# Optimization experiments

Measured on AMD Instinct MI355X. Metric: run time of the kernel, lower is better.

Reference implementation:

```python
import jax, jax.numpy as jnp
import numpy as np

C = 64
D = C // 8  # query/key channels
B, H, W = 4, 64, 64


def setup_inputs() -> dict:
    key = jax.random.key(0)
    ks = jax.random.split(key, 8)
    x = jax.random.normal(ks[0], (B, C, H, W), dtype=jnp.float32)
    # 1x1 conv params (kernel squeezed to [out_ch, in_ch])
    sq = 1.0 / np.sqrt(C)
    Wq = jax.random.uniform(ks[1], (D, C), jnp.float32, -sq, sq)
    bq = jax.random.uniform(ks[2], (D,), jnp.float32, -sq, sq)
    Wk = jax.random.uniform(ks[3], (D, C), jnp.float32, -sq, sq)
    bk = jax.random.uniform(ks[4], (D,), jnp.float32, -sq, sq)
    Wv = jax.random.uniform(ks[5], (C, C), jnp.float32, -sq, sq)
    bv = jax.random.uniform(ks[6], (C,), jnp.float32, -sq, sq)
    # gamma is zero-initialized in the module; use a nonzero value so the
    # attention path actually contributes to the output.
    gamma = jax.random.normal(ks[7], (1,), dtype=jnp.float32)
    return {"x": x, "Wq": Wq, "bq": bq, "Wk": Wk, "bk": bk, "Wv": Wv, "bv": bv, "gamma": gamma}


def reference(x, Wq, bq, Wk, bk, Wv, bv, gamma):
    b, c, h, w = x.shape
    n = h * w
    xf = x.reshape(b, c, n)                                   # [B,C,N]
    q = jnp.einsum('dc,bcn->bdn', Wq, xf) + bq[None, :, None]  # [B,D,N]
    k = jnp.einsum('dc,bcn->bdn', Wk, xf) + bk[None, :, None]  # [B,D,N]
    v = jnp.einsum('ec,bcn->ben', Wv, xf) + bv[None, :, None]  # [B,C,N]
    energy = jnp.einsum('bdn,bdm->bnm', q, k)                  # [B,N,N] = Q^T K
    attn = jax.nn.softmax(energy, axis=-1)                     # softmax over keys m
    # out[b,c,n] = sum_m v[b,c,m] * attn[b,n,m]  (V @ attention^T in torch)
    out = jnp.einsum('bcm,bnm->bcn', v, attn).reshape(b, c, h, w)
    return gamma[0] * out + x
```

## Files before the change

### kernel.cpp

```cpp
#include <hip/hip_runtime.h>
#include <hip/hip_bf16.h>
#include <math.h>

#define BB 4
#define CC 64
#define DD 8
#define NN 4096
#define KS 8
#define KPS (NN / KS)
#define LOG2E 1.44269504088896340736f

typedef __attribute__((ext_vector_type(4))) short short4v;
typedef __attribute__((ext_vector_type(8))) unsigned short ushort8;
typedef __attribute__((ext_vector_type(16))) float f32x16;

#if defined(__HIP_DEVICE_COMPILE__)
  #if __has_builtin(__builtin_amdgcn_mfma_f32_32x32x8bf16_1k)
    #define MFMA32x8(A, B, C) __builtin_amdgcn_mfma_f32_32x32x8bf16_1k(A, B, C, 0, 0, 0)
  #elif __has_builtin(__builtin_amdgcn_mfma_f32_32x32x8_bf16)
    #define MFMA32x8(A, B, C) __builtin_amdgcn_mfma_f32_32x32x8_bf16(A, B, C, 0, 0, 0)
  #else
    #error "no 32x32x8 bf16 MFMA builtin in device pass"
  #endif
  #if __has_builtin(__builtin_amdgcn_exp2f)
    #define EXP2(x) __builtin_amdgcn_exp2f(x)
  #else
    #define EXP2(x) exp2f(x)
  #endif
#else
  static __device__ __host__ inline f32x16 MFMA32x8(short4v, short4v, f32x16 c) { return c; }
  #define EXP2(x) exp2f(x)
#endif

static __device__ inline short4v pack4(float a, float b, float c, float d) {
    union { short4v s; __hip_bfloat162 h[2]; } u;
    u.h[0] = __float22bfloat162_rn(make_float2(a, b));
    u.h[1] = __float22bfloat162_rn(make_float2(c, d));
    return u.s;
}

__global__ __launch_bounds__(256) void qkv_kernel(
    const float* __restrict__ x,  const float* __restrict__ Wq, const float* __restrict__ bq,
    const float* __restrict__ Wk, const float* __restrict__ bk,
    const float* __restrict__ Wv, const float* __restrict__ bv,
    unsigned short* __restrict__ qb, unsigned short* __restrict__ kb,
    unsigned short* __restrict__ vT)
{
    __shared__ unsigned short LQ[128 * 8];
    __shared__ unsigned short LK[128 * 8];

    int tid = threadIdx.x;
    int wave = tid >> 6, lane = tid & 63;
    int l32 = lane & 31, h2 = lane >> 5;

    int blk = blockIdx.x;
    int b = blk & (BB - 1);
    int r2 = blk >> 2;
    int rt = r2 % 3;
    int ng = r2 / 3;
    int n0 = ng * 128 + wave * 32;

    short4v af[8];
    #pragma unroll
    for (int s = 0; s < 8; ++s) {
        float4 w4;
        if (rt < 2) {
            w4 = *(const float4*)(Wv + (size_t)(rt * 32 + l32) * CC + s * 8 + 4 * h2);
        } else if (l32 < 8) {
            w4 = *(const float4*)(Wq + (size_t)l32 * CC + s * 8 + 4 * h2);
        } else if (l32 < 16) {
            w4 = *(const float4*)(Wk + (size_t)(l32 - 8) * CC + s * 8 + 4 * h2);
        } else {
            w4 = make_float4(0.f, 0.f, 0.f, 0.f);
        }
        af[s] = pack4(w4.x, w4.y, w4.z, w4.w);
    }

    const float* xb = x + (size_t)b * CC * NN + n0 + l32;
    short4v bf[8];
    #pragma unroll
    for (int s = 0; s < 8; ++s) {
        int c0 = s * 8 + 4 * h2;
        float x0 = xb[(size_t)(c0 + 0) * NN];
        float x1 = xb[(size_t)(c0 + 1) * NN];
        float x2 = xb[(size_t)(c0 + 2) * NN];
        float x3 = xb[(size_t)(c0 + 3) * NN];
        bf[s] = pack4(x0, x1, x2, x3);
    }

    f32x16 acc;
    #pragma unroll
    for (int r = 0; r < 16; ++r) acc[r] = 0.f;
    #pragma unroll
    for (int s = 0; s < 8; ++s)
        acc = MFMA32x8(af[s], bf[s], acc);

    if (rt < 2) {
        #pragma unroll
        for (int r = 0; r < 16; ++r) {
            int row = rt * 32 + (r & 3) + 8 * (r >> 2) + 4 * h2;
            float val = acc[r] + bv[row];
            __hip_bfloat16 hv = __float2bfloat16(val);
            vT[((size_t)b * CC + row) * NN + n0 + l32] = *(unsigned short*)&hv;
        }
    } else {
        short4v qp = pack4((acc[0] + bq[0 + 4 * h2]) * LOG2E,
                           (acc[1] + bq[1 + 4 * h2]) * LOG2E,
                           (acc[2] + bq[2 + 4 * h2]) * LOG2E,
                           (acc[3] + bq[3 + 4 * h2]) * LOG2E);
        short4v kp = pack4(acc[4] + bk[0 + 4 * h2],
                           acc[5] + bk[1 + 4 * h2],
                           acc[6] + bk[2 + 4 * h2],
                           acc[7] + bk[3 + 4 * h2]);
        int nl = wave * 32 + l32;
        *(short4v*)(LQ + (size_t)nl * 8 + 4 * h2) = qp;
        *(short4v*)(LK + (size_t)nl * 8 + 4 * h2) = kp;
        __syncthreads();
        if (tid < 128) {
            ushort8 row = *(const ushort8*)(LQ + (size_t)tid * 8);
            *(ushort8*)(qb + ((size_t)b * NN + ng * 128 + tid) * 8) = row;
        } else {
            int t = tid - 128;
            ushort8 row = *(const ushort8*)(LK + (size_t)t * 8);
            *(ushort8*)(kb + ((size_t)b * NN + ng * 128 + t) * 8) = row;
        }
    }
}

__global__ __launch_bounds__(256, 4) void flash_kernel(
    const unsigned short* __restrict__ qb, const unsigned short* __restrict__ kb,
    const unsigned short* __restrict__ vT, float* __restrict__ obuf,
    float* __restrict__ ssb)
{
    __shared__ unsigned short VS[64 * 132];
    int tid = threadIdx.x;
    int wave = tid >> 6, lane = tid & 63;
    int l32 = lane & 31, h2 = lane >> 5;

    int blk = blockIdx.x;
    int b = blk & (BB - 1);
    int rest = blk >> 2;
    int split = rest & (KS - 1);
    int qchunk = rest >> 3;
    int n0 = qchunk * 128 + wave * 32;

    short4v qf = *(const short4v*)(qb + ((size_t)b * NN + n0 + l32) * DD + h2 * 4);

    const unsigned short* kbb = kb + (size_t)b * NN * DD;
    const unsigned short* vbb = vT + (size_t)b * CC * NN;
    int m0 = split * KPS;

    int cch = tid >> 4, kg = tid & 15;
    int kgx = (kg ^ (cch & 3)) * 8;

    f32x16 o0, o1, zz;
    #pragma unroll
    for (int r = 0; r < 16; ++r) { o0[r] = 0.f; o1[r] = 0.f; zz[r] = 0.f; }
    float s0 = 0.f, s1 = 0.f, s2 = 0.f, s3 = 0.f;

    ushort8 vr0 = *(const ushort8*)(vbb + (size_t)(cch)      * NN + m0 + kg * 8);
    ushort8 vr1 = *(const ushort8*)(vbb + (size_t)(16 + cch) * NN + m0 + kg * 8);
    ushort8 vr2 = *(const ushort8*)(vbb + (size_t)(32 + cch) * NN + m0 + kg * 8);
    ushort8 vr3 = *(const ushort8*)(vbb + (size_t)(48 + cch) * NN + m0 + kg * 8);

    for (int tile = 0; tile < 4; ++tile) {
        *(ushort8*)(VS + (size_t)(cch)      * 132 + kgx) = vr0;
        *(ushort8*)(VS + (size_t)(16 + cch) * 132 + kgx) = vr1;
        *(ushort8*)(VS + (size_t)(32 + cch) * 132 + kgx) = vr2;
        *(ushort8*)(VS + (size_t)(48 + cch) * 132 + kgx) = vr3;
        __syncthreads();

        if (tile < 3) {
            int mn = m0 + (tile + 1) * 128;
            vr0 = *(const ushort8*)(vbb + (size_t)(cch)      * NN + mn + kg * 8);
            vr1 = *(const ushort8*)(vbb + (size_t)(16 + cch) * NN + mn + kg * 8);
            vr2 = *(const ushort8*)(vbb + (size_t)(32 + cch) * NN + mn + kg * 8);
            vr3 = *(const ushort8*)(vbb + (size_t)(48 + cch) * NN + mn + kg * 8);
        }

        short4v kf[4];
        #pragma unroll
        for (int s = 0; s < 4; ++s)
            kf[s] = *(const short4v*)(kbb + (size_t)(m0 + tile * 128 + s * 32 + l32) * DD + h2 * 4);

        #pragma unroll
        for (int sub = 0; sub < 4; ++sub) {
            f32x16 st = MFMA32x8(kf[sub], qf, zz);
            float w[16];
            #pragma unroll
            for (int r = 0; r < 16; ++r) w[r] = EXP2(st[r]);
            s0 += (w[0] + w[1]) + (w[2] + w[3]);
            s1 += (w[4] + w[5]) + (w[6] + w[7]);
            s2 += (w[8] + w[9]) + (w[10] + w[11]);
            s3 += (w[12] + w[13]) + (w[14] + w[15]);

            union { short4v s; __hip_bfloat162 h[2]; } u[4];
            #pragma unroll
            for (int g = 0; g < 4; ++g) {
                u[g].h[0] = __float22bfloat162_rn(make_float2(w[4 * g],     w[4 * g + 1]));
                u[g].h[1] = __float22bfloat162_rn(make_float2(w[4 * g + 2], w[4 * g + 3]));
            }
            #pragma unroll
            for (int g = 0; g < 4; ++g) {
                int go = ((sub * 4 + g) ^ (l32 & 3)) * 8 + h2 * 4;
                short4v vf0 = *(const short4v*)(VS + (size_t)(l32)      * 132 + go);
                short4v vf1 = *(const short4v*)(VS + (size_t)(32 + l32) * 132 + go);
                o0 = MFMA32x8(u[g].s, vf0, o0);
                o1 = MFMA32x8(u[g].s, vf1, o1);
            }
        }
        __syncthreads();
    }

    float* ob = obuf + ((size_t)(b * NN + n0)) * CC;
    #pragma unroll
    for (int r = 0; r < 16; ++r) {
        int qrow = (r & 3) + 8 * (r >> 2) + 4 * h2;
        unsafeAtomicAdd(ob + (size_t)qrow * CC + l32,      o0[r]);
        unsafeAtomicAdd(ob + (size_t)qrow * CC + 32 + l32, o1[r]);
    }
    float ssum = (s0 + s1) + (s2 + s3);
    ssum += __shfl_xor(ssum, 32);
    if (lane < 32)
        unsafeAtomicAdd(ssb + (size_t)b * NN + n0 + l32, ssum);
}

__global__ __launch_bounds__(256) void norm_kernel(
    const float* __restrict__ obuf, const float* __restrict__ ssb,
    const float* __restrict__ x, const float* __restrict__ gamma,
    float* __restrict__ out)
{
    __shared__ float tile[32 * 65];
    __shared__ float stl[32];
    int blk = blockIdx.x;
    int b = blk >> 7;
    int n0 = (blk & 127) * 32;
    int tid = threadIdx.x;

    if (tid < 32) stl[tid] = 1.0f / ssb[(size_t)b * NN + n0 + tid];

    int nl = tid >> 4, cg = tid & 15;
    #pragma unroll
    for (int p = 0; p < 2; ++p) {
        int n = p * 16 + nl;
        float4 v = *(const float4*)(obuf + ((size_t)(b * NN + n0 + n)) * CC + cg * 4);
        tile[n * 65 + cg * 4 + 0] = v.x;
        tile[n * 65 + cg * 4 + 1] = v.y;
        tile[n * 65 + cg * 4 + 2] = v.z;
        tile[n * 65 + cg * 4 + 3] = v.w;
    }
    __syncthreads();
    float g = gamma[0];
    #pragma unroll
    for (int p = 0; p < 8; ++p) {
        int idx = p * 256 + tid;
        int c = idx >> 5, n_l = idx & 31;
        size_t xi = ((size_t)b * CC + c) * NN + n0 + n_l;
        out[xi] = g * tile[n_l * 65 + c] * stl[n_l] + x[xi];
    }
}

extern "C" void kernel_launch(void* const* d_in, const int* in_sizes, int n_in,
                              void* d_out, int out_size, void* d_ws, size_t ws_size,
                              hipStream_t stream)
{
    const float* x     = (const float*)d_in[0];
    const float* Wq    = (const float*)d_in[1];
    const float* bq    = (const float*)d_in[2];
    const float* Wk    = (const float*)d_in[3];
    const float* bk    = (const float*)d_in[4];
    const float* Wv    = (const float*)d_in[5];
    const float* bv    = (const float*)d_in[6];
    const float* gamma = (const float*)d_in[7];
    float* out = (float*)d_out;

    float* ws = (float*)d_ws;
    size_t off = 0;
    unsigned short* qb = (unsigned short*)(ws + off); off += (size_t)BB * NN * DD / 2 + 64;
    unsigned short* kb = (unsigned short*)(ws + off); off += (size_t)BB * NN * DD / 2 + 64;
    unsigned short* vT = (unsigned short*)(ws + off); off += (size_t)BB * CC * NN / 2 + 64;
    float* obuf = ws + off; off += (size_t)BB * NN * CC;
    float* ssb  = ws + off; off += (size_t)BB * NN;

    hipMemsetAsync(obuf, 0, ((size_t)BB * NN * CC + (size_t)BB * NN) * sizeof(float), stream);

    qkv_kernel<<<BB * 3 * 32, 256, 0, stream>>>(x, Wq, bq, Wk, bk, Wv, bv, qb, kb, vT);
    flash_kernel<<<BB * (NN / 128) * KS, 256, 0, stream>>>(qb, kb, vT, obuf, ssb);
    norm_kernel<<<BB * 128, 256, 0, stream>>>(obuf, ssb, x, gamma, out);
}
```

Before: 114.8 us.

## Replace atomic split-K reduction with bf16 partial buffers and double-buffered V tiles

Halves the key-split count and makes each flash block write its partial output and row sums to a private bf16/fp32 slot, with no atomics. The norm kernel then reduces those slots, which also removes the memset. The V tile in shared memory is double-buffered and the next K fragments are prefetched, so one barrier per tile is enough and loads overlap with compute. The cost is lower precision in the partial accumulators (bf16) and fewer blocks in the flash kernel, which may reduce occupancy across the CUs.

```diff
diff --git a/kernel.cpp b/kernel.cpp
--- a/kernel.cpp
+++ b/kernel.cpp
@@ -6,8 +6,9 @@
 #define CC 64
 #define DD 8
 #define NN 4096
-#define KS 8
+#define KS 4
 #define KPS (NN / KS)
+#define NT  (KPS / 128)
 #define LOG2E 1.44269504088896340736f
 
 typedef __attribute__((ext_vector_type(4))) short short4v;
@@ -129,10 +130,10 @@
 
 __global__ __launch_bounds__(256, 4) void flash_kernel(
     const unsigned short* __restrict__ qb, const unsigned short* __restrict__ kb,
-    const unsigned short* __restrict__ vT, float* __restrict__ obuf,
-    float* __restrict__ ssb)
+    const unsigned short* __restrict__ vT, unsigned short* __restrict__ accb,
+    float* __restrict__ sbuf)
 {
-    __shared__ unsigned short VS[64 * 132];
+    __shared__ unsigned short VS[2][64 * 132];
     int tid = threadIdx.x;
     int wave = tid >> 6, lane = tid & 63;
     int l32 = lane & 31, h2 = lane >> 5;
@@ -141,7 +142,7 @@
     int b = blk & (BB - 1);
     int rest = blk >> 2;
     int split = rest & (KS - 1);
-    int qchunk = rest >> 3;
+    int qchunk = rest >> 2;
     int n0 = qchunk * 128 + wave * 32;
 
     short4v qf = *(const short4v*)(qb + ((size_t)b * NN + n0 + l32) * DD + h2 * 4);
@@ -158,31 +159,34 @@
     for (int r = 0; r < 16; ++r) { o0[r] = 0.f; o1[r] = 0.f; zz[r] = 0.f; }
     float s0 = 0.f, s1 = 0.f, s2 = 0.f, s3 = 0.f;
 
-    ushort8 vr0 = *(const ushort8*)(vbb + (size_t)(cch)      * NN + m0 + kg * 8);
-    ushort8 vr1 = *(const ushort8*)(vbb + (size_t)(16 + cch) * NN + m0 + kg * 8);
-    ushort8 vr2 = *(const ushort8*)(vbb + (size_t)(32 + cch) * NN + m0 + kg * 8);
-    ushort8 vr3 = *(const ushort8*)(vbb + (size_t)(48 + cch) * NN + m0 + kg * 8);
-
-    for (int tile = 0; tile < 4; ++tile) {
-        *(ushort8*)(VS + (size_t)(cch)      * 132 + kgx) = vr0;
-        *(ushort8*)(VS + (size_t)(16 + cch) * 132 + kgx) = vr1;
-        *(ushort8*)(VS + (size_t)(32 + cch) * 132 + kgx) = vr2;
-        *(ushort8*)(VS + (size_t)(48 + cch) * 132 + kgx) = vr3;
+    short4v kf[4];
+    #pragma unroll
+    for (int s = 0; s < 4; ++s)
+        kf[s] = *(const short4v*)(kbb + (size_t)(m0 + s * 32 + l32) * DD + h2 * 4);
+    ushort8 w0 = *(const ushort8*)(vbb + (size_t)(cch)      * NN + m0 + kg * 8);
+    ushort8 w1 = *(const ushort8*)(vbb + (size_t)(16 + cch) * NN + m0 + kg * 8);
+    ushort8 w2 = *(const ushort8*)(vbb + (size_t)(32 + cch) * NN + m0 + kg * 8);
+    ushort8 w3 = *(const ushort8*)(vbb + (size_t)(48 + cch) * NN + m0 + kg * 8);
+    *(ushort8*)(VS[0] + (size_t)(cch)      * 132 + kgx) = w0;
+    *(ushort8*)(VS[0] + (size_t)(16 + cch) * 132 + kgx) = w1;
+    *(ushort8*)(VS[0] + (size_t)(32 + cch) * 132 + kgx) = w2;
+    *(ushort8*)(VS[0] + (size_t)(48 + cch) * 132 + kgx) = w3;
+
+    int buf = 0;
+    for (int tile = 0; tile < NT; ++tile) {
         __syncthreads();
 
-        if (tile < 3) {
-            int mn = m0 + (tile + 1) * 128;
-            vr0 = *(const ushort8*)(vbb + (size_t)(cch)      * NN + mn + kg * 8);
-            vr1 = *(const ushort8*)(vbb + (size_t)(16 + cch) * NN + mn + kg * 8);
-            vr2 = *(const ushort8*)(vbb + (size_t)(32 + cch) * NN + mn + kg * 8);
-            vr3 = *(const ushort8*)(vbb + (size_t)(48 + cch) * NN + mn + kg * 8);
-        }
-
-        short4v kf[4];
+        int mn = m0 + (tile + 1) * 128;
+        short4v kn[4];
         #pragma unroll
         for (int s = 0; s < 4; ++s)
-            kf[s] = *(const short4v*)(kbb + (size_t)(m0 + tile * 128 + s * 32 + l32) * DD + h2 * 4);
-
+            kn[s] = *(const short4v*)(kbb + (size_t)(mn + s * 32 + l32) * DD + h2 * 4);
+        w0 = *(const ushort8*)(vbb + (size_t)(cch)      * NN + mn + kg * 8);
+        w1 = *(const ushort8*)(vbb + (size_t)(16 + cch) * NN + mn + kg * 8);
+        w2 = *(const ushort8*)(vbb + (size_t)(32 + cch) * NN + mn + kg * 8);
+        w3 = *(const ushort8*)(vbb + (size_t)(48 + cch) * NN + mn + kg * 8);
+
+        const unsigned short* Vb = VS[buf];
         #pragma unroll
         for (int sub = 0; sub < 4; ++sub) {
             f32x16 st = MFMA32x8(kf[sub], qf, zz);
@@ -203,30 +207,40 @@
             #pragma unroll
             for (int g = 0; g < 4; ++g) {
                 int go = ((sub * 4 + g) ^ (l32 & 3)) * 8 + h2 * 4;
-                short4v vf0 = *(const short4v*)(VS + (size_t)(l32)      * 132 + go);
-                short4v vf1 = *(const short4v*)(VS + (size_t)(32 + l32) * 132 + go);
+                short4v vf0 = *(const short4v*)(Vb + (size_t)(l32)      * 132 + go);
+                short4v vf1 = *(const short4v*)(Vb + (size_t)(32 + l32) * 132 + go);
                 o0 = MFMA32x8(u[g].s, vf0, o0);
                 o1 = MFMA32x8(u[g].s, vf1, o1);
             }
         }
-        __syncthreads();
-    }
-
-    float* ob = obuf + ((size_t)(b * NN + n0)) * CC;
+
+        if (tile != NT - 1) {
+            unsigned short* Vn = VS[buf ^ 1];
+            *(ushort8*)(Vn + (size_t)(cch)      * 132 + kgx) = w0;
+            *(ushort8*)(Vn + (size_t)(16 + cch) * 132 + kgx) = w1;
+            *(ushort8*)(Vn + (size_t)(32 + cch) * 132 + kgx) = w2;
+            *(ushort8*)(Vn + (size_t)(48 + cch) * 132 + kgx) = w3;
+            #pragma unroll
+            for (int s = 0; s < 4; ++s) kf[s] = kn[s];
+        }
+        buf ^= 1;
+    }
+
+    __hip_bfloat16* ab = (__hip_bfloat16*)accb + (((size_t)(b * KS + split)) * NN + n0) * CC;
     #pragma unroll
     for (int r = 0; r < 16; ++r) {
         int qrow = (r & 3) + 8 * (r >> 2) + 4 * h2;
-        unsafeAtomicAdd(ob + (size_t)qrow * CC + l32,      o0[r]);
-        unsafeAtomicAdd(ob + (size_t)qrow * CC + 32 + l32, o1[r]);
+        ab[(size_t)qrow * CC + l32]      = __float2bfloat16(o0[r]);
+        ab[(size_t)qrow * CC + 32 + l32] = __float2bfloat16(o1[r]);
     }
     float ssum = (s0 + s1) + (s2 + s3);
     ssum += __shfl_xor(ssum, 32);
     if (lane < 32)
-        unsafeAtomicAdd(ssb + (size_t)b * NN + n0 + l32, ssum);
+        sbuf[(size_t)(b * KS + split) * NN + n0 + l32] = ssum;
 }
 
 __global__ __launch_bounds__(256) void norm_kernel(
-    const float* __restrict__ obuf, const float* __restrict__ ssb,
+    const unsigned short* __restrict__ accb, const float* __restrict__ sbuf,
     const float* __restrict__ x, const float* __restrict__ gamma,
     float* __restrict__ out)
 {
@@ -237,19 +251,30 @@
     int n0 = (blk & 127) * 32;
     int tid = threadIdx.x;
 
-    if (tid < 32) stl[tid] = 1.0f / ssb[(size_t)b * NN + n0 + tid];
-
-    int nl = tid >> 4, cg = tid & 15;
-    #pragma unroll
-    for (int p = 0; p < 2; ++p) {
-        int n = p * 16 + nl;
-        float4 v = *(const float4*)(obuf + ((size_t)(b * NN + n0 + n)) * CC + cg * 4);
-        tile[n * 65 + cg * 4 + 0] = v.x;
-        tile[n * 65 + cg * 4 + 1] = v.y;
-        tile[n * 65 + cg * 4 + 2] = v.z;
-        tile[n * 65 + cg * 4 + 3] = v.w;
-    }
+    if (tid < 32) {
+        float st = 0.f;
+        #pragma unroll
+        for (int sp = 0; sp < KS; ++sp)
+            st += sbuf[(size_t)(b * KS + sp) * NN + n0 + tid];
+        stl[tid] = 1.0f / st;
+    }
+
+    int nl = tid >> 3, cg = tid & 7;
+    float a[8];
+    #pragma unroll
+    for (int e = 0; e < 8; ++e) a[e] = 0.f;
+    #pragma unroll
+    for (int sp = 0; sp < KS; ++sp) {
+        ushort8 v = *(const ushort8*)(accb + (((size_t)(b * KS + sp) * NN) + n0 + nl) * CC + cg * 8);
+        #pragma unroll
+        for (int e = 0; e < 8; ++e)
+            a[e] += __uint_as_float(((unsigned)v[e]) << 16);
+    }
+    #pragma unroll
+    for (int e = 0; e < 8; ++e)
+        tile[nl * 65 + cg * 8 + e] = a[e];
     __syncthreads();
+
     float g = gamma[0];
     #pragma unroll
     for (int p = 0; p < 8; ++p) {
@@ -279,12 +304,10 @@
     unsigned short* qb = (unsigned short*)(ws + off); off += (size_t)BB * NN * DD / 2 + 64;
     unsigned short* kb = (unsigned short*)(ws + off); off += (size_t)BB * NN * DD / 2 + 64;
     unsigned short* vT = (unsigned short*)(ws + off); off += (size_t)BB * CC * NN / 2 + 64;
-    float* obuf = ws + off; off += (size_t)BB * NN * CC;
-    float* ssb  = ws + off; off += (size_t)BB * NN;
-
-    hipMemsetAsync(obuf, 0, ((size_t)BB * NN * CC + (size_t)BB * NN) * sizeof(float), stream);
+    unsigned short* accb = (unsigned short*)(ws + off); off += (size_t)BB * KS * NN * CC / 2 + 64;
+    float* sbuf = ws + off; off += (size_t)BB * KS * NN;
 
     qkv_kernel<<<BB * 3 * 32, 256, 0, stream>>>(x, Wq, bq, Wk, bk, Wv, bv, qb, kb, vT);
-    flash_kernel<<<BB * (NN / 128) * KS, 256, 0, stream>>>(qb, kb, vT, obuf, ssb);
-    norm_kernel<<<BB * 128, 256, 0, stream>>>(obuf, ssb, x, gamma, out);
-}
+    flash_kernel<<<BB * (NN / 128) * KS, 256, 0, stream>>>(qb, kb, vT, accb, sbuf);
+    norm_kernel<<<BB * 128, 256, 0, stream>>>(accb, sbuf, x, gamma, out);
+}
```

New measurement: 110.4 us. 3.8% less time.
